# Kernel tuning notes

Measured on AMD Instinct MI355X. Metric: run time of the kernel, lower is better.

Reference implementation:

```python
import jax, jax.numpy as jnp
import numpy as np

N_EMBD = 1024
N_HEAD = 16
HEAD_DIM = N_EMBD // N_HEAD
B, T = 2, 2048
EPS = 1e-5


def setup_inputs() -> dict:
    key = jax.random.key(0)
    ks = jax.random.split(key, 12)
    s = lambda fan_in: 1.0 / np.sqrt(fan_in)
    return {
        "x": jax.random.normal(ks[0], (B, T, N_EMBD), dtype=jnp.float32),
        "ln1_g": jnp.ones((N_EMBD,), jnp.float32),
        "ln1_b": jnp.zeros((N_EMBD,), jnp.float32),
        "W_attn": jax.random.normal(ks[1], (N_EMBD, 3 * N_EMBD), jnp.float32) * s(N_EMBD),
        "b_attn": jnp.zeros((3 * N_EMBD,), jnp.float32),
        "W_proj": jax.random.normal(ks[2], (N_EMBD, N_EMBD), jnp.float32) * s(N_EMBD),
        "b_proj": jnp.zeros((N_EMBD,), jnp.float32),
        "ln2_g": jnp.ones((N_EMBD,), jnp.float32),
        "ln2_b": jnp.zeros((N_EMBD,), jnp.float32),
        "W_fc": jax.random.normal(ks[3], (N_EMBD, 4 * N_EMBD), jnp.float32) * s(N_EMBD),
        "b_fc": jnp.zeros((4 * N_EMBD,), jnp.float32),
        "W_fc2": jax.random.normal(ks[4], (4 * N_EMBD, N_EMBD), jnp.float32) * s(4 * N_EMBD),
        "b_fc2": jnp.zeros((N_EMBD,), jnp.float32),
    }


def _layernorm(x, g, b):
    mu = jnp.mean(x, axis=-1, keepdims=True)
    var = jnp.mean(jnp.square(x - mu), axis=-1, keepdims=True)
    return (x - mu) * jax.lax.rsqrt(var + EPS) * g + b


def _attention(x, W_attn, b_attn, W_proj, b_proj):
    Bsz, Tlen, C = x.shape
    qkv = x @ W_attn + b_attn  # [B,T,3C]
    q, k, v = jnp.split(qkv, 3, axis=-1)
    # [B,H,T,D]
    q = q.reshape(Bsz, Tlen, N_HEAD, HEAD_DIM).transpose(0, 2, 1, 3)
    k = k.reshape(Bsz, Tlen, N_HEAD, HEAD_DIM).transpose(0, 2, 1, 3)
    v = v.reshape(Bsz, Tlen, N_HEAD, HEAD_DIM).transpose(0, 2, 1, 3)
    att = jnp.einsum("bhqd,bhkd->bhqk", q, k) * (HEAD_DIM ** -0.5)
    causal = jnp.tril(jnp.ones((Tlen, Tlen), dtype=bool))
    att = jnp.where(causal[None, None], att, -jnp.inf)
    att = jax.nn.softmax(att, axis=-1)
    y = jnp.einsum("bhqk,bhkd->bhqd", att, v)
    y = y.transpose(0, 2, 1, 3).reshape(Bsz, Tlen, C)
    return y @ W_proj + b_proj


def _mlp(x, W_fc, b_fc, W_fc2, b_fc2):
    h = jax.nn.gelu(x @ W_fc + b_fc, approximate=False)
    return h @ W_fc2 + b_fc2


def reference(x, ln1_g, ln1_b, W_attn, b_attn, W_proj, b_proj,
              ln2_g, ln2_b, W_fc, b_fc, W_fc2, b_fc2):
    x = x + _attention(_layernorm(x, ln1_g, ln1_b), W_attn, b_attn, W_proj, b_proj)
    x = x + _mlp(_layernorm(x, ln2_g, ln2_b), W_fc, b_fc, W_fc2, b_fc2)
    return x
```

## Files before the change

### kernel.cpp

```cpp
#include <hip/hip_runtime.h>
#include <math.h>

typedef unsigned short ushort_t;
typedef __attribute__((ext_vector_type(8))) short f16x8;
typedef __attribute__((ext_vector_type(4))) float f32x4;

#define N_EMBD 1024
#define N_HEAD 16
#define HEAD_DIM 64
#define SEQ_B 2
#define SEQ_T 2048
#define M_TOK (SEQ_B * SEQ_T)

__device__ __forceinline__ ushort_t f2b(float f) {
    union { float f; unsigned int u; } v; v.f = f;
    unsigned int r = (v.u + 0x7FFFu + ((v.u >> 16) & 1u)) >> 16;
    return (ushort_t)r;
}

__device__ __forceinline__ float gelu_fast(float v) {
    float u = v + 0.044715f * v * v * v;
    float e = __expf(-1.5957691216057308f * u);
    return v * __frcp_rn(1.0f + e);
}

__device__ __forceinline__ void gload_lds16(const ushort_t* g, ushort_t* l) {
    __builtin_amdgcn_global_load_lds(
        (const __attribute__((address_space(1))) void*)g,
        (__attribute__((address_space(3))) void*)l, 16, 0, 0);
}

__global__ __launch_bounds__(256) void prep_w(
    const float* __restrict__ Wa, const float* __restrict__ Wp,
    const float* __restrict__ Wf, const float* __restrict__ Wf2,
    ushort_t* __restrict__ Ta, ushort_t* __restrict__ Tp,
    ushort_t* __restrict__ Tf, ushort_t* __restrict__ Tf2,
    const float* __restrict__ x, const float* __restrict__ g1,
    const float* __restrict__ b1, ushort_t* __restrict__ xn) {
    int b = blockIdx.x;
    int t = threadIdx.x;
    if (b >= 12288) {
        int row = b - 12288;
        const float4 v = ((const float4*)(x + (size_t)row * N_EMBD))[t];
        float s = v.x + v.y + v.z + v.w;
        float s2 = v.x * v.x + v.y * v.y + v.z * v.z + v.w * v.w;
        for (int m = 1; m < 64; m <<= 1) {
            s += __shfl_xor(s, m, 64);
            s2 += __shfl_xor(s2, m, 64);
        }
        __shared__ float ss[4], ss2[4];
        if ((t & 63) == 0) { ss[t >> 6] = s; ss2[t >> 6] = s2; }
        __syncthreads();
        s = ss[0] + ss[1] + ss[2] + ss[3];
        s2 = ss2[0] + ss2[1] + ss2[2] + ss2[3];
        float mu = s * (1.0f / N_EMBD);
        float var = s2 * (1.0f / N_EMBD) - mu * mu;
        float rs = rsqrtf(var + 1e-5f);
        const float4 gg = ((const float4*)g1)[t];
        const float4 bb = ((const float4*)b1)[t];
        ushort_t o4[4];
        o4[0] = f2b((v.x - mu) * rs * gg.x + bb.x);
        o4[1] = f2b((v.y - mu) * rs * gg.y + bb.y);
        o4[2] = f2b((v.z - mu) * rs * gg.z + bb.z);
        o4[3] = f2b((v.w - mu) * rs * gg.w + bb.w);
        *(ushort4*)(xn + (size_t)row * N_EMBD + t * 4) = *(ushort4*)o4;
        return;
    }
    __shared__ float tile[32][33];
    const float* W; ushort_t* T; int K, N, nx;
    if (b < 3072)      { W = Wa;  T = Ta;  K = 1024; N = 3072; nx = 96; }
    else if (b < 4096) { W = Wp;  T = Tp;  K = 1024; N = 1024; nx = 32; b -= 3072; }
    else if (b < 8192) { W = Wf;  T = Tf;  K = 1024; N = 4096; nx = 128; b -= 4096; }
    else               { W = Wf2; T = Tf2; K = 4096; N = 1024; nx = 32; b -= 8192; }
    int n0 = (b % nx) * 32, k0 = (b / nx) * 32;
    for (int i = 0; i < 4; ++i) {
        int l = t + i * 256; int r = l >> 5, c2 = l & 31;
        tile[r][c2] = W[(size_t)(k0 + r) * N + n0 + c2];
    }
    __syncthreads();
    for (int i = 0; i < 4; ++i) {
        int l = t + i * 256; int r = l >> 5, c2 = l & 31;
        T[(size_t)(n0 + r) * K + k0 + c2] = f2b(tile[c2][r]);
    }
}

__global__ __launch_bounds__(256) void ln2_kernel(
    const float* __restrict__ x, const float* __restrict__ g,
    const float* __restrict__ b, ushort_t* __restrict__ out) {
    int row = blockIdx.x;
    int t = threadIdx.x;
    const float4 v = ((const float4*)(x + (size_t)row * N_EMBD))[t];
    float s = v.x + v.y + v.z + v.w;
    float s2 = v.x * v.x + v.y * v.y + v.z * v.z + v.w * v.w;
    for (int m = 1; m < 64; m <<= 1) {
        s += __shfl_xor(s, m, 64);
        s2 += __shfl_xor(s2, m, 64);
    }
    __shared__ float ss[4], ss2[4];
    if ((t & 63) == 0) { ss[t >> 6] = s; ss2[t >> 6] = s2; }
    __syncthreads();
    s = ss[0] + ss[1] + ss[2] + ss[3];
    s2 = ss2[0] + ss2[1] + ss2[2] + ss2[3];
    float mu = s * (1.0f / N_EMBD);
    float var = s2 * (1.0f / N_EMBD) - mu * mu;
    float rs = rsqrtf(var + 1e-5f);
    const float4 gg = ((const float4*)g)[t];
    const float4 bb = ((const float4*)b)[t];
    ushort_t o4[4];
    o4[0] = f2b((v.x - mu) * rs * gg.x + bb.x);
    o4[1] = f2b((v.y - mu) * rs * gg.y + bb.y);
    o4[2] = f2b((v.z - mu) * rs * gg.z + bb.z);
    o4[3] = f2b((v.w - mu) * rs * gg.w + bb.w);
    *(ushort4*)(out + (size_t)row * N_EMBD + t * 4) = *(ushort4*)o4;
}

template <int MODE, int NJ>
__device__ __forceinline__ void gemm_epilogue(
    f32x4 (&acc)[4][NJ], const float* __restrict__ bias,
    const float* __restrict__ resid, void* __restrict__ Cout,
    int m0, int n0, int wr, int wc, int quad, int l16, int N) {
    for (int i = 0; i < 4; ++i) {
        for (int j = 0; j < NJ; ++j) {
            int col = n0 + wc + j * 16 + l16;
            float bv = bias[col];
            for (int r = 0; r < 4; ++r) {
                int row = m0 + wr + i * 16 + quad * 4 + r;
                float v = acc[i][j][r] + bv;
                if (MODE == 2) v = gelu_fast(v);
                if (MODE == 1 || MODE == 3) v += resid[(size_t)row * N + col];
                if (MODE == 0 || MODE == 2)
                    ((ushort_t*)Cout)[(size_t)row * N + col] = f2b(v);
                else
                    ((float*)Cout)[(size_t)row * N + col] = v;
            }
        }
    }
}

template <int MODE>
__device__ __forceinline__ void gemm_body_dma(
    const ushort_t* __restrict__ A, const ushort_t* __restrict__ Bt,
    const float* __restrict__ bias, const float* __restrict__ resid,
    void* __restrict__ Cout, int M, int N, int K) {
    __shared__ ushort_t As[2][128 * 32];
    __shared__ ushort_t Bs[2][128 * 32];
    int t = threadIdx.x;
    int wave = t >> 6, lane = t & 63;
    int quad = lane >> 4, l16 = lane & 15;
    const int swl = (l16 ^ (l16 >> 2)) & 3;
    int wr = (wave >> 1) * 64, wc = (wave & 1) * 64;
    const int m0 = blockIdx.y * 128, n0 = blockIdx.x * 128;

    const int c = wave * 64 + lane;
    const int srow = c >> 2, s_l = c & 3;
    const int s_g = s_l ^ ((srow ^ (srow >> 2)) & 3);
    const ushort_t* Ap = &A[(size_t)(m0 + srow) * K + s_g * 8];
    const ushort_t* Bp = &Bt[(size_t)(n0 + srow) * K + s_g * 8];

    const int NK = K >> 5;
    gload_lds16(Ap, &As[0][wave * 512]);
    gload_lds16(Ap + (size_t)64 * K, &As[0][wave * 512 + 2048]);
    gload_lds16(Bp, &Bs[0][wave * 512]);
    gload_lds16(Bp + (size_t)64 * K, &Bs[0][wave * 512 + 2048]);

    f32x4 acc[4][4] = {};
    for (int kt = 0; kt < NK; ++kt) {
        const int cur = kt & 1;
        __syncthreads();
        if (kt + 1 < NK) {
            const int nxt = cur ^ 1;
            const int k0 = (kt + 1) << 5;
            gload_lds16(Ap + k0, &As[nxt][wave * 512]);
            gload_lds16(Ap + (size_t)64 * K + k0, &As[nxt][wave * 512 + 2048]);
            gload_lds16(Bp + k0, &Bs[nxt][wave * 512]);
            gload_lds16(Bp + (size_t)64 * K + k0, &Bs[nxt][wave * 512 + 2048]);
        }
        f16x8 af[4], bf[4];
        for (int i = 0; i < 4; ++i)
            af[i] = *(const f16x8*)&As[cur][(wr + i * 16 + l16) * 32 + (quad ^ swl) * 8];
        for (int j = 0; j < 4; ++j)
            bf[j] = *(const f16x8*)&Bs[cur][(wc + j * 16 + l16) * 32 + (quad ^ swl) * 8];
        for (int i = 0; i < 4; ++i)
            for (int j = 0; j < 4; ++j)
                acc[i][j] = __builtin_amdgcn_mfma_f32_16x16x32_bf16(
                    af[i], bf[j], acc[i][j], 0, 0, 0);
    }
    gemm_epilogue<MODE, 4>(acc, bias, resid, Cout, m0, n0, wr, wc, quad, l16, N);
}

__global__ __launch_bounds__(256) void gemm_mlp1(
    const ushort_t* A, const ushort_t* Bt, const float* bias, void* C,
    int M, int N, int K) { gemm_body_dma<2>(A, Bt, bias, nullptr, C, M, N, K); }

template <int GATE, bool DA, bool DB>
__device__ __forceinline__ void tile4(
    f32x4 (&acc)[8][4],
    const ushort_t* __restrict__ Ah,
    const ushort_t* __restrict__ Bh,
    int rB, int l16, int quad, int sw, int K,
    const ushort_t* gA, ushort_t* lA,
    const ushort_t* gB, ushort_t* lB)
{
    const int s0 = (quad ^ sw) << 3, s1 = ((4 | quad) ^ sw) << 3;
    f16x8 bfr[4][2];
#pragma unroll
    for (int j = 0; j < 4; ++j) {
        const ushort_t* p = &Bh[(rB + j * 16 + l16) * 64];
        bfr[j][0] = *(const f16x8*)(p + s0);
        bfr[j][1] = *(const f16x8*)(p + s1);
    }
#pragma unroll
    for (int ph = 0; ph < 4; ++ph) {
        f16x8 a[2][2];
#pragma unroll
        for (int r = 0; r < 2; ++r) {
            const ushort_t* p = &Ah[((ph * 2 + r) * 16 + l16) * 64];
            a[r][0] = *(const f16x8*)(p + s0);
            a[r][1] = *(const f16x8*)(p + s1);
        }
        if (DA && ph < 2) {
            const ushort_t* g = gA + (size_t)(ph * 128) * K;
            ushort_t* l = lA + ph * 8192;
            gload_lds16(g, l);
            gload_lds16(g + (size_t)64 * K, l + 4096);
        }
        if (DB && ph >= 2) {
            const ushort_t* g = gB + (size_t)((ph - 2) * 128) * K;
            ushort_t* l = lB + (ph - 2) * 8192;
            gload_lds16(g, l);
            gload_lds16(g + (size_t)64 * K, l + 4096);
        }
        asm volatile("s_barrier" ::: "memory");
        __builtin_amdgcn_s_setprio(1);
#pragma unroll
        for (int r = 0; r < 2; ++r)
#pragma unroll
            for (int j = 0; j < 4; ++j) {
                acc[ph * 2 + r][j] = __builtin_amdgcn_mfma_f32_16x16x32_bf16(
                    a[r][0], bfr[j][0], acc[ph * 2 + r][j], 0, 0, 0);
                acc[ph * 2 + r][j] = __builtin_amdgcn_mfma_f32_16x16x32_bf16(
                    a[r][1], bfr[j][1], acc[ph * 2 + r][j], 0, 0, 0);
            }
        __builtin_amdgcn_s_setprio(0);
        if (ph < 3)
            asm volatile("s_waitcnt lgkmcnt(0)\n\ts_barrier" ::: "memory");
        else if (GATE == 1)
            asm volatile("s_waitcnt vmcnt(4) lgkmcnt(0)\n\ts_barrier" ::: "memory");
        else if (GATE == 2)
            asm volatile("s_waitcnt vmcnt(0) lgkmcnt(0)\n\ts_barrier" ::: "memory");
        else
            asm volatile("s_waitcnt lgkmcnt(0)\n\ts_barrier" ::: "memory");
    }
}

template <int MODE>
__global__ __launch_bounds__(512) void gemm256(
    const ushort_t* __restrict__ A, const ushort_t* __restrict__ Bt,
    const float* __restrict__ bias, ushort_t* __restrict__ C,
    int M, int N, int K) {
    __shared__ ushort_t As[2][2][8192];
    __shared__ ushort_t Bs[2][2][8192];
    const int t = threadIdx.x, w = t >> 6, lane = t & 63;
    const int quad = lane >> 4, l16 = lane & 15, sw = l16 & 7;
    const int wm = w >> 2, wn = w & 3;
    const int m0 = blockIdx.y * 256, n0 = blockIdx.x * 256;
    const int r8 = lane >> 3, g8 = (lane & 7) ^ r8;
    const ushort_t* Aln = A + (size_t)(m0 + w * 8 + r8) * K + g8 * 8;
    const ushort_t* Bln = Bt + (size_t)(n0 + w * 8 + r8) * K + g8 * 8;
    ushort_t* sA0 = &As[0][0][w * 512];
    ushort_t* sA1 = &As[1][0][w * 512];
    ushort_t* sB0 = &Bs[0][0][w * 512];
    ushort_t* sB1 = &Bs[1][0][w * 512];
    const ushort_t* Ah0 = &As[0][wm][0];
    const ushort_t* Ah1 = &As[1][wm][0];
    const ushort_t* Bh0 = &Bs[0][wn >> 1][0];
    const ushort_t* Bh1 = &Bs[1][wn >> 1][0];
    const int rB = (wn & 1) * 64;

#define STAGE_HALF(gln, tk, h, ldsbase)                                      \
    do {                                                                     \
        const ushort_t* _g = (gln) + (size_t)(h) * 128 * K + (tk) * 64;      \
        ushort_t* _l = (ldsbase) + (h) * 8192;                               \
        gload_lds16(_g, _l);                                                 \
        gload_lds16(_g + (size_t)64 * K, _l + 4096);                         \
    } while (0)

    STAGE_HALF(Aln, 0, 0, sA0); STAGE_HALF(Aln, 0, 1, sA0);
    STAGE_HALF(Bln, 0, 0, sB0); STAGE_HALF(Bln, 0, 1, sB0);
    STAGE_HALF(Bln, 1, 0, sB1); STAGE_HALF(Bln, 1, 1, sB1);
    asm volatile("s_waitcnt vmcnt(4) lgkmcnt(0)\n\ts_barrier" ::: "memory");
#undef STAGE_HALF

    f32x4 acc[8][4] = {};
    const int NP = (K >> 7) - 1;
    for (int it = 0; it < NP; ++it) {
        const int U = 2 * it;
        tile4<1, true, true>(acc, Ah0, Bh0, rB, l16, quad, sw, K,
                             Aln + (U + 1) * 64, sA1, Bln + (U + 2) * 64, sB0);
        tile4<1, true, true>(acc, Ah1, Bh1, rB, l16, quad, sw, K,
                             Aln + (U + 2) * 64, sA0, Bln + (U + 3) * 64, sB1);
    }
    {
        const int U = 2 * NP;
        tile4<2, true, false>(acc, Ah0, Bh0, rB, l16, quad, sw, K,
                              Aln + (U + 1) * 64, sA1, nullptr, nullptr);
        tile4<0, false, false>(acc, Ah1, Bh1, rB, l16, quad, sw, K,
                               nullptr, nullptr, nullptr, nullptr);
    }

#pragma unroll
    for (int mi = 0; mi < 8; ++mi)
#pragma unroll
        for (int nj = 0; nj < 4; ++nj) {
            int col = n0 + wn * 64 + nj * 16 + l16;
            float bv = bias[col];
#pragma unroll
            for (int r = 0; r < 4; ++r) {
                int row = m0 + wm * 128 + mi * 16 + quad * 4 + r;
                float v = acc[mi][nj][r] + bv;
                if (MODE == 2) v = gelu_fast(v);
                C[(size_t)row * N + col] = f2b(v);
            }
        }
}

template <int MODE>
__device__ __forceinline__ void gemm_body_splitk(
    const ushort_t* __restrict__ A, const ushort_t* __restrict__ Bt,
    const float* __restrict__ bias, const float* __restrict__ resid,
    void* __restrict__ Cout, int M, int N, int K) {
    __shared__ ushort_t As[2][2][128 * 32];
    __shared__ ushort_t Bs[2][2][64 * 32];
    int t = threadIdx.x;
    int wave = t >> 6, lane = t & 63;
    int half = wave >> 2, w4 = wave & 3;
    int quad = lane >> 4, l16 = lane & 15;
    const int swl = (l16 ^ (l16 >> 2)) & 3;
    int wr = (w4 >> 1) * 64, wc = (w4 & 1) * 32;
    const int m0 = blockIdx.y * 128, n0 = blockIdx.x * 64;

    const int K2 = K >> 1;
    const int c = w4 * 64 + lane;
    const int srow = c >> 2, s_l = c & 3;
    const int s_g = s_l ^ ((srow ^ (srow >> 2)) & 3);
    const ushort_t* Ap = &A[(size_t)(m0 + srow) * K + (size_t)half * K2 + s_g * 8];
    const ushort_t* Bp = &Bt[(size_t)(n0 + srow) * K + (size_t)half * K2 + s_g * 8];

    const int NK = K2 >> 5;
    gload_lds16(Ap, &As[0][half][w4 * 512]);
    gload_lds16(Ap + (size_t)64 * K, &As[0][half][w4 * 512 + 2048]);
    gload_lds16(Bp, &Bs[0][half][w4 * 512]);

    f32x4 acc[4][2] = {};
    for (int kt = 0; kt < NK; ++kt) {
        const int cur = kt & 1;
        __syncthreads();
        if (kt + 1 < NK) {
            const int nxt = cur ^ 1;
            const int k0 = (kt + 1) << 5;
            gload_lds16(Ap + k0, &As[nxt][half][w4 * 512]);
            gload_lds16(Ap + (size_t)64 * K + k0, &As[nxt][half][w4 * 512 + 2048]);
            gload_lds16(Bp + k0, &Bs[nxt][half][w4 * 512]);
        }
        f16x8 af[4], bf[2];
        for (int i = 0; i < 4; ++i)
            af[i] = *(const f16x8*)&As[cur][half][(wr + i * 16 + l16) * 32 + (quad ^ swl) * 8];
        for (int j = 0; j < 2; ++j)
            bf[j] = *(const f16x8*)&Bs[cur][half][(wc + j * 16 + l16) * 32 + (quad ^ swl) * 8];
        for (int i = 0; i < 4; ++i)
            for (int j = 0; j < 2; ++j)
                acc[i][j] = __builtin_amdgcn_mfma_f32_16x16x32_bf16(
                    af[i], bf[j], acc[i][j], 0, 0, 0);
    }
    __syncthreads();
    float* red = (float*)&As[0][0][0];
    if (half == 1) {
        for (int i = 0; i < 4; ++i)
            for (int j = 0; j < 2; ++j)
                for (int r = 0; r < 4; ++r)
                    red[(wr + i * 16 + quad * 4 + r) * 64 + wc + j * 16 + l16] =
                        acc[i][j][r];
    }
    __syncthreads();
    if (half == 0) {
        for (int i = 0; i < 4; ++i)
            for (int j = 0; j < 2; ++j)
                for (int r = 0; r < 4; ++r)
                    acc[i][j][r] +=
                        red[(wr + i * 16 + quad * 4 + r) * 64 + wc + j * 16 + l16];
        gemm_epilogue<MODE, 2>(acc, bias, resid, Cout, m0, n0, wr, wc, quad, l16, N);
    }
}

__global__ __launch_bounds__(512) void gemm_proj(
    const ushort_t* A, const ushort_t* Bt, const float* bias,
    const float* resid, void* C, int M, int N, int K) {
    gemm_body_splitk<1>(A, Bt, bias, resid, C, M, N, K); }
__global__ __launch_bounds__(512) void gemm_out(
    const ushort_t* A, const ushort_t* Bt, const float* bias,
    const float* resid, void* C, int M, int N, int K) {
    gemm_body_splitk<3>(A, Bt, bias, resid, C, M, N, K); }

__global__ __launch_bounds__(256) void attn_kernel(
    const ushort_t* __restrict__ qkv, ushort_t* __restrict__ y) {
    const int bh = blockIdx.y;
    const int b = bh >> 4, h = bh & 15;
    const int tok0 = b * SEQ_T;
    const int t = threadIdx.x, wave = t >> 6, lane = t & 63;
    const int quad = lane >> 4, l16 = lane & 15;
    const int sw8 = l16 & 7;
    const size_t ld = 3 * N_EMBD;
    const ushort_t* Qb = qkv + (size_t)tok0 * ld + h * HEAD_DIM;
    const ushort_t* Kb = Qb + N_EMBD;
    const ushort_t* Vb = Qb + 2 * N_EMBD;

    __shared__ ushort_t Ks[2][128 * 64];
    __shared__ ushort_t Vt[64 * 136];
    __shared__ ushort_t Pl[4][16 * 128];

    const int kc = wave * 64 + lane;
    const int kv_s = kc >> 3, ks_l = kc & 7;
    const int ks_g = ks_l ^ (kv_s & 7);
    const ushort_t* KpL = Kb + (size_t)kv_s * ld + ks_g * 8;

    const int v_dcI = t & 7, v_dc = v_dcI * 8;
    int v_kv[4], v_pos[4];
    for (int i = 0; i < 4; ++i) {
        int l = t + i * 256;
        v_kv[i] = l >> 3;
        v_pos[i] = v_kv[i] ^ (v_dcI << 3);
    }

    f16x8 onesB;
    for (int i = 0; i < 8; ++i) onesB[i] = (short)0x3F80;

    for (int phase = 0; phase < 2; ++phase) {
        const int qt = phase == 0 ? (int)blockIdx.x : 31 - (int)blockIdx.x;
        const int q0 = qt * 64;
        const int nkt = (q0 + 191) >> 7;

        const int qrow = q0 + wave * 16 + l16;
        f16x8 qf0 = *(const f16x8*)&Qb[(size_t)qrow * ld + quad * 8];
        f16x8 qf1 = *(const f16x8*)&Qb[(size_t)qrow * ld + 32 + quad * 8];

        f32x4 o[4] = {};
        f32x4 lsum = {};

        __syncthreads();
        gload_lds16(KpL, &Ks[0][wave * 512]);
        gload_lds16(KpL + (size_t)32 * ld, &Ks[0][wave * 512 + 2048]);
        gload_lds16(KpL + (size_t)64 * ld, &Ks[0][wave * 512 + 4096]);
        gload_lds16(KpL + (size_t)96 * ld, &Ks[0][wave * 512 + 6144]);
        for (int i = 0; i < 4; ++i) {
            uint4 r = *(const uint4*)&Vb[(size_t)v_kv[i] * ld + v_dc];
            const ushort_t* pv = (const ushort_t*)&r;
            for (int e = 0; e < 8; ++e)
                Vt[(v_dc + e) * 136 + v_pos[i]] = pv[e];
        }

        for (int kt = 0; kt < nkt; ++kt) {
            const int cur = kt & 1;
            __syncthreads();
            const bool pf = (kt + 1 < nkt);
            uint4 vr[4];
            if (pf) {
                for (int i = 0; i < 4; ++i)
                    vr[i] = *(const uint4*)&Vb[(size_t)((kt + 1) * 128 + v_kv[i]) * ld + v_dc];
                const ushort_t* kp = KpL + (size_t)(kt + 1) * 128 * ld;
                gload_lds16(kp, &Ks[cur ^ 1][wave * 512]);
                gload_lds16(kp + (size_t)32 * ld, &Ks[cur ^ 1][wave * 512 + 2048]);
                gload_lds16(kp + (size_t)64 * ld, &Ks[cur ^ 1][wave * 512 + 4096]);
                gload_lds16(kp + (size_t)96 * ld, &Ks[cur ^ 1][wave * 512 + 6144]);
            }
            f32x4 s[8];
            const int ksl = (quad ^ sw8) << 3;
            __builtin_amdgcn_s_setprio(1);
            for (int j = 0; j < 8; ++j) {
                const int kr = j * 16 + l16;
                f16x8 kf0 = *(const f16x8*)&Ks[cur][kr * 64 + ksl];
                f16x8 kf1 = *(const f16x8*)&Ks[cur][kr * 64 + (ksl ^ 32)];
                f32x4 z = {};
                z = __builtin_amdgcn_mfma_f32_16x16x32_bf16(qf0, kf0, z, 0, 0, 0);
                z = __builtin_amdgcn_mfma_f32_16x16x32_bf16(qf1, kf1, z, 0, 0, 0);
                s[j] = z;
            }
            __builtin_amdgcn_s_setprio(0);
            if (kt == nkt - 1) {
                const int qg = q0 + wave * 16 + quad * 4;
                for (int j = 0; j < 8; ++j) {
                    int kg = kt * 128 + j * 16 + l16;
                    for (int r = 0; r < 4; ++r)
                        if (kg > qg + r) s[j][r] = -INFINITY;
                }
            }
            ushort_t* myP = Pl[wave];
            for (int j = 0; j < 8; ++j) {
                int kvv = j * 16 + l16;
                int chunk = kvv >> 3, klo = kvv & 7;
                for (int r = 0; r < 4; ++r) {
                    float p = __expf(__builtin_fmaf(s[j][r], 0.125f, -20.0f));
                    int q = quad * 4 + r;
                    myP[q * 128 + ((chunk ^ (q & 7)) << 3) + klo] = f2b(p);
                }
            }
            f16x8 pa[4];
            for (int ks = 0; ks < 4; ++ks)
                pa[ks] = *(const f16x8*)&myP[l16 * 128 + ((((ks << 2) | quad) ^ sw8) << 3)];
            __builtin_amdgcn_s_setprio(1);
            for (int ks = 0; ks < 4; ++ks)
                lsum = __builtin_amdgcn_mfma_f32_16x16x32_bf16(pa[ks], onesB, lsum, 0, 0, 0);
            for (int dj = 0; dj < 4; ++dj) {
                const int d = dj * 16 + l16;
                const int dsw3 = (d >> 3) & 7;
                f32x4 oo = o[dj];
                for (int ks = 0; ks < 4; ++ks) {
                    f16x8 vb = *(const f16x8*)&Vt[d * 136 + ((((ks << 2) | quad) ^ dsw3) << 3)];
                    oo = __builtin_amdgcn_mfma_f32_16x16x32_bf16(pa[ks], vb, oo, 0, 0, 0);
                }
                o[dj] = oo;
            }
            __builtin_amdgcn_s_setprio(0);
            if (pf) {
                asm volatile("s_barrier" ::: "memory");
                for (int i = 0; i < 4; ++i) {
                    const ushort_t* pv = (const ushort_t*)&vr[i];
                    for (int e = 0; e < 8; ++e)
                        Vt[(v_dc + e) * 136 + v_pos[i]] = pv[e];
                }
            }
        }
        float rl[4];
        for (int r = 0; r < 4; ++r) rl[r] = __frcp_rn(lsum[r]);
        for (int dj = 0; dj < 4; ++dj)
            for (int r = 0; r < 4; ++r) {
                int row = tok0 + q0 + wave * 16 + quad * 4 + r;
                int col = h * HEAD_DIM + dj * 16 + l16;
                y[(size_t)row * N_EMBD + col] = f2b(o[dj][r] * rl[r]);
            }
    }
}

extern "C" void kernel_launch(void* const* d_in, const int* in_sizes, int n_in,
                              void* d_out, int out_size, void* d_ws, size_t ws_size,
                              hipStream_t stream) {
    const float* x      = (const float*)d_in[0];
    const float* ln1_g  = (const float*)d_in[1];
    const float* ln1_b  = (const float*)d_in[2];
    const float* W_attn = (const float*)d_in[3];
    const float* b_attn = (const float*)d_in[4];
    const float* W_proj = (const float*)d_in[5];
    const float* b_proj = (const float*)d_in[6];
    const float* ln2_g  = (const float*)d_in[7];
    const float* ln2_b  = (const float*)d_in[8];
    const float* W_fc   = (const float*)d_in[9];
    const float* b_fc   = (const float*)d_in[10];
    const float* W_fc2  = (const float*)d_in[11];
    const float* b_fc2  = (const float*)d_in[12];
    float* out = (float*)d_out;

    char* w = (char*)d_ws;
    size_t o = 0;
    ushort_t* xn      = (ushort_t*)(w + o); o += (size_t)M_TOK * N_EMBD * 2;
    ushort_t* qkv     = (ushort_t*)(w + o); o += (size_t)M_TOK * 3 * N_EMBD * 2;
    ushort_t* y       = (ushort_t*)(w + o); o += (size_t)M_TOK * N_EMBD * 2;
    float*    x1      = (float*)(w + o);    o += (size_t)M_TOK * N_EMBD * 4;
    ushort_t* x1n     = (ushort_t*)(w + o); o += (size_t)M_TOK * N_EMBD * 2;
    ushort_t* hbuf    = (ushort_t*)(w + o); o += (size_t)M_TOK * 4 * N_EMBD * 2;
    ushort_t* Wt_attn = (ushort_t*)(w + o); o += (size_t)N_EMBD * 3 * N_EMBD * 2;
    ushort_t* Wt_proj = (ushort_t*)(w + o); o += (size_t)N_EMBD * N_EMBD * 2;
    ushort_t* Wt_fc   = (ushort_t*)(w + o); o += (size_t)N_EMBD * 4 * N_EMBD * 2;
    ushort_t* Wt_fc2  = (ushort_t*)(w + o); o += (size_t)4 * N_EMBD * N_EMBD * 2;

    prep_w<<<12288 + M_TOK, 256, 0, stream>>>(
        W_attn, W_proj, W_fc, W_fc2, Wt_attn, Wt_proj, Wt_fc, Wt_fc2,
        x, ln1_g, ln1_b, xn);
    gemm256<0><<<dim3(3 * N_EMBD / 256, M_TOK / 256), 512, 0, stream>>>(
        xn, Wt_attn, b_attn, qkv, M_TOK, 3 * N_EMBD, N_EMBD);
    attn_kernel<<<dim3(SEQ_T / 128, SEQ_B * N_HEAD), 256, 0, stream>>>(qkv, y);
    gemm_proj<<<dim3(N_EMBD / 64, M_TOK / 128), 512, 0, stream>>>(
        y, Wt_proj, b_proj, x, x1, M_TOK, N_EMBD, N_EMBD);
    ln2_kernel<<<M_TOK, 256, 0, stream>>>(x1, ln2_g, ln2_b, x1n);
    gemm_mlp1<<<dim3(4 * N_EMBD / 128, M_TOK / 128), 256, 0, stream>>>(
        x1n, Wt_fc, b_fc, hbuf, M_TOK, 4 * N_EMBD, N_EMBD);
    gemm_out<<<dim3(N_EMBD / 64, M_TOK / 128), 512, 0, stream>>>(
        hbuf, Wt_fc2, b_fc2, x1, out, M_TOK, N_EMBD, 4 * N_EMBD);
    (void)in_sizes; (void)n_in; (void)out_size; (void)ws_size;
}
```

Baseline: 363.1 us.

## Split-K GEMMs: K-step 64, B fragments straight to registers, fewer barriers

The split-K GEMM used for the projection and output layers now processes 64 K-elements per step, staging two 32-wide A slices into LDS per step. The B operand is loaded directly from global memory into registers instead of going through LDS. This halves the number of barriers per K and drops B's LDS traffic, at the cost of uncoalesced per-lane global loads for B and more registers. The loop is unrolled by two with ping-pong buffers, and it assumes NK2 is even.

```diff
diff --git a/kernel.cpp b/kernel.cpp
--- a/kernel.cpp
+++ b/kernel.cpp
@@ -325,12 +325,11 @@
 }
 
 template <int MODE>
-__device__ __forceinline__ void gemm_body_splitk(
+__device__ __forceinline__ void gemm_body_splitk64(
     const ushort_t* __restrict__ A, const ushort_t* __restrict__ Bt,
     const float* __restrict__ bias, const float* __restrict__ resid,
     void* __restrict__ Cout, int M, int N, int K) {
-    __shared__ ushort_t As[2][2][128 * 32];
-    __shared__ ushort_t Bs[2][2][64 * 32];
+    __shared__ ushort_t As[2][2][2][128 * 32];
     int t = threadIdx.x;
     int wave = t >> 6, lane = t & 63;
     int half = wave >> 2, w4 = wave & 3;
@@ -344,36 +343,66 @@
     const int srow = c >> 2, s_l = c & 3;
     const int s_g = s_l ^ ((srow ^ (srow >> 2)) & 3);
     const ushort_t* Ap = &A[(size_t)(m0 + srow) * K + (size_t)half * K2 + s_g * 8];
-    const ushort_t* Bp = &Bt[(size_t)(n0 + srow) * K + (size_t)half * K2 + s_g * 8];
-
-    const int NK = K2 >> 5;
-    gload_lds16(Ap, &As[0][half][w4 * 512]);
-    gload_lds16(Ap + (size_t)64 * K, &As[0][half][w4 * 512 + 2048]);
-    gload_lds16(Bp, &Bs[0][half][w4 * 512]);
+    const ushort_t* Bp = &Bt[(size_t)(n0 + wc + l16) * K + (size_t)half * K2 + quad * 8];
+
+    const int NK2 = K2 >> 6;
+
+    f16x8 bf0[2][2], bf1[2][2];
+
+#define STAGE_A64(kt, buf)                                                    \
+    do {                                                                      \
+        const int _k0 = (kt) << 6;                                            \
+        _Pragma("unroll")                                                     \
+        for (int _ks = 0; _ks < 2; ++_ks) {                                   \
+            gload_lds16(Ap + _k0 + _ks * 32, &As[buf][half][_ks][w4 * 512]);  \
+            gload_lds16(Ap + (size_t)64 * K + _k0 + _ks * 32,                 \
+                        &As[buf][half][_ks][w4 * 512 + 2048]);                \
+        }                                                                     \
+    } while (0)
+
+#define LOAD_B64(kt, bf)                                                      \
+    do {                                                                      \
+        const int _k0 = (kt) << 6;                                            \
+        _Pragma("unroll")                                                     \
+        for (int _j = 0; _j < 2; ++_j)                                        \
+            _Pragma("unroll")                                                 \
+            for (int _ks = 0; _ks < 2; ++_ks)                                 \
+                bf[_j][_ks] = *(const f16x8*)(Bp + (size_t)_j * 16 * K +      \
+                                              _k0 + _ks * 32);                \
+    } while (0)
+
+#define MFMA_T64(buf, bf)                                                     \
+    do {                                                                      \
+        _Pragma("unroll")                                                     \
+        for (int _ks = 0; _ks < 2; ++_ks)                                     \
+            _Pragma("unroll")                                                 \
+            for (int _i = 0; _i < 4; ++_i) {                                  \
+                f16x8 _af = *(const f16x8*)&As[buf][half][_ks]                \
+                    [(wr + _i * 16 + l16) * 32 + (quad ^ swl) * 8];           \
+                _Pragma("unroll")                                             \
+                for (int _j = 0; _j < 2; ++_j)                                \
+                    acc[_i][_j] = __builtin_amdgcn_mfma_f32_16x16x32_bf16(    \
+                        _af, bf[_j][_ks], acc[_i][_j], 0, 0, 0);              \
+            }                                                                 \
+    } while (0)
 
     f32x4 acc[4][2] = {};
-    for (int kt = 0; kt < NK; ++kt) {
-        const int cur = kt & 1;
+    STAGE_A64(0, 0);
+    LOAD_B64(0, bf0);
+    for (int it = 0; it < NK2; it += 2) {
         __syncthreads();
-        if (kt + 1 < NK) {
-            const int nxt = cur ^ 1;
-            const int k0 = (kt + 1) << 5;
-            gload_lds16(Ap + k0, &As[nxt][half][w4 * 512]);
-            gload_lds16(Ap + (size_t)64 * K + k0, &As[nxt][half][w4 * 512 + 2048]);
-            gload_lds16(Bp + k0, &Bs[nxt][half][w4 * 512]);
-        }
-        f16x8 af[4], bf[2];
-        for (int i = 0; i < 4; ++i)
-            af[i] = *(const f16x8*)&As[cur][half][(wr + i * 16 + l16) * 32 + (quad ^ swl) * 8];
-        for (int j = 0; j < 2; ++j)
-            bf[j] = *(const f16x8*)&Bs[cur][half][(wc + j * 16 + l16) * 32 + (quad ^ swl) * 8];
-        for (int i = 0; i < 4; ++i)
-            for (int j = 0; j < 2; ++j)
-                acc[i][j] = __builtin_amdgcn_mfma_f32_16x16x32_bf16(
-                    af[i], bf[j], acc[i][j], 0, 0, 0);
-    }
+        if (it + 1 < NK2) { STAGE_A64(it + 1, 1); LOAD_B64(it + 1, bf1); }
+        MFMA_T64(0, bf0);
+        __syncthreads();
+        if (it + 2 < NK2) { STAGE_A64(it + 2, 0); LOAD_B64(it + 2, bf0); }
+        MFMA_T64(1, bf1);
+    }
+#undef STAGE_A64
+#undef LOAD_B64
+#undef MFMA_T64
+
     __syncthreads();
-    float* red = (float*)&As[0][0][0];
+    float* red = (float*)&As[0][0][0][0];
     if (half == 1) {
         for (int i = 0; i < 4; ++i)
             for (int j = 0; j < 2; ++j)
@@ -395,11 +424,11 @@
 __global__ __launch_bounds__(512) void gemm_proj(
     const ushort_t* A, const ushort_t* Bt, const float* bias,
     const float* resid, void* C, int M, int N, int K) {
-    gemm_body_splitk<1>(A, Bt, bias, resid, C, M, N, K); }
+    gemm_body_splitk64<1>(A, Bt, bias, resid, C, M, N, K); }
 __global__ __launch_bounds__(512) void gemm_out(
     const ushort_t* A, const ushort_t* Bt, const float* bias,
     const float* resid, void* C, int M, int N, int K) {
-    gemm_body_splitk<3>(A, Bt, bias, resid, C, M, N, K); }
+    gemm_body_splitk64<3>(A, Bt, bias, resid, C, M, N, K); }
 
 __global__ __launch_bounds__(256) void attn_kernel(
     const ushort_t* __restrict__ qkv, ushort_t* __restrict__ y) {
```

Result: slower. 395.3 us (+8.9%).
